# Kernel optimization log

Measured on AMD Instinct MI355X. Metric: run time of the kernel, lower is better.

## Reference

```python
import jax, jax.numpy as jnp
import numpy as np

NU = 100000  # user nodes
NI = 100000  # item nodes
NE = 600000  # edges per etype


def mean_agg(Wh, src, dst, n_dst):
    # copy_u + mean reduce: gather projected src feats, segment-mean over dst
    msg = Wh[src]                                               # [E, d]
    s = jax.ops.segment_sum(msg, dst, num_segments=n_dst)       # [n_dst, d]
    deg = jax.ops.segment_sum(jnp.ones((src.shape[0],), Wh.dtype), dst,
                              num_segments=n_dst)               # [n_dst]
    return s / jnp.maximum(deg, 1.0)[:, None]                   # isolated nodes -> 0


def setup_inputs() -> dict:
    key = jax.random.key(0)
    ks = jax.random.split(key, 20)
    d_in, d_hid, d_out = 128, 128, 16
    inp = {
        'embed_user': jax.random.normal(ks[0], (NU, d_in), jnp.float32),
        'embed_item': jax.random.normal(ks[1], (NI, d_in), jnp.float32),
        'src_uu': jax.random.randint(ks[2], (NE,), 0, NU, jnp.int32),
        'dst_uu': jax.random.randint(ks[3], (NE,), 0, NU, jnp.int32),
        'src_ui': jax.random.randint(ks[4], (NE,), 0, NU, jnp.int32),
        'dst_ui': jax.random.randint(ks[5], (NE,), 0, NI, jnp.int32),
        'src_iu': jax.random.randint(ks[6], (NE,), 0, NI, jnp.int32),
        'dst_iu': jax.random.randint(ks[7], (NE,), 0, NU, jnp.int32),
        'W0_uu': jax.random.normal(ks[8], (d_in, d_hid), jnp.float32) * 0.05,
        'b0_uu': jax.random.normal(ks[9], (d_hid,), jnp.float32) * 0.05,
        'W0_ui': jax.random.normal(ks[10], (d_in, d_hid), jnp.float32) * 0.05,
        'b0_ui': jax.random.normal(ks[11], (d_hid,), jnp.float32) * 0.05,
        'W0_iu': jax.random.normal(ks[12], (d_in, d_hid), jnp.float32) * 0.05,
        'b0_iu': jax.random.normal(ks[13], (d_hid,), jnp.float32) * 0.05,
        'W1_uu': jax.random.normal(ks[14], (d_hid, d_out), jnp.float32) * 0.05,
        'b1_uu': jax.random.normal(ks[15], (d_out,), jnp.float32) * 0.05,
        'W1_ui': jax.random.normal(ks[16], (d_hid, d_out), jnp.float32) * 0.05,
        'b1_ui': jax.random.normal(ks[17], (d_out,), jnp.float32) * 0.05,
        'W1_iu': jax.random.normal(ks[18], (d_hid, d_out), jnp.float32) * 0.05,
        'b1_iu': jax.random.normal(ks[19], (d_out,), jnp.float32) * 0.05,
    }
    return inp


def reference(embed_user, embed_item,
              src_uu, dst_uu, src_ui, dst_ui, src_iu, dst_iu,
              W0_uu, b0_uu, W0_ui, b0_ui, W0_iu, b0_iu,
              W1_uu, b1_uu, W1_ui, b1_ui, W1_iu, b1_iu):
    # Layer 0: per-etype linear, copy_u+mean per etype, sum-combine per dst ntype
    h_user = (mean_agg(embed_user @ W0_uu + b0_uu, src_uu, dst_uu, NU)
              + mean_agg(embed_item @ W0_iu + b0_iu, src_iu, dst_iu, NU))
    h_item = mean_agg(embed_user @ W0_ui + b0_ui, src_ui, dst_ui, NI)
    h_user = jax.nn.relu(h_user)
    h_item = jax.nn.relu(h_item)
    # Layer 1 (dropout p=0): only category='user' output is returned
    out = (mean_agg(h_user @ W1_uu + b1_uu, src_uu, dst_uu, NU)
           + mean_agg(h_item @ W1_iu + b1_iu, src_iu, dst_iu, NU))
    return out
```

## Files before the change

kernel.cpp:

```cpp
#include <hip/hip_runtime.h>
#include <hip/hip_bf16.h>

#define NU 100000
#define NI 100000
#define NEDGE 600000
#define DIN 128
#define DOUT 16
#define NPAD 100032
#define BSH 9
#define NBUCK 196
#define NSB 256
#define SCH 2344

typedef __attribute__((ext_vector_type(8))) short short8;
typedef __attribute__((ext_vector_type(4))) float f32x4;

#define W_EU   0ull
#define W_AUI  6400000ull
#define W_AUU  12802048ull
#define W_AIU  19204096ull
#define W_PW   25606144ull
#define W_OFFU 25632768ull
#define W_OFFI 25732784ull
#define W_OFFX 25832800ull
#define W_SUU  25932816ull
#define W_SIU  26532816ull
#define W_SUI  27132816ull
#define W_EI   27732944ull
#define WS_FULL_BYTES (34132944ull * 4)

__device__ inline unsigned pack_bf16(float x, float y) {
  __hip_bfloat162 h = __float22bfloat162_rn(make_float2(x, y));
  unsigned u;
  __builtin_memcpy(&u, &h, 4);
  return u;
}

__device__ inline short bf16_bits(float x) {
  __hip_bfloat16 h = __float2bfloat16(x);
  short s;
  __builtin_memcpy(&s, &h, 2);
  return s;
}

__device__ inline void bf2_accw(unsigned u, float w, float& ax, float& ay) {
  unsigned lo = u << 16, hi = u & 0xffff0000u;
  float f0, f1;
  __builtin_memcpy(&f0, &lo, 4);
  __builtin_memcpy(&f1, &hi, 4);
  ax = fmaf(f0, w, ax);
  ay = fmaf(f1, w, ay);
}

__global__ __launch_bounds__(256) void prep_kernel(
    const float* __restrict__ Eu, const float* __restrict__ Ei,
    unsigned* __restrict__ Eu_b, unsigned* __restrict__ Ei_b,
    const int* __restrict__ d_uu, const int* __restrict__ d_iu, const int* __restrict__ d_ui,
    int* __restrict__ M,
    const float* __restrict__ W0_uu, const float* __restrict__ W0_ui,
    const float* __restrict__ W0_iu, const float* __restrict__ W1_uu,
    const float* __restrict__ W1_iu, short* __restrict__ pW0_uu, short* __restrict__ pW0_ui,
    short* __restrict__ pW0_iu, short* __restrict__ pW1_uu, short* __restrict__ pW1_iu,
    int nconvU, int nconvI) {
  __shared__ int h[NBUCK];
  int b = blockIdx.x;
  int tid = threadIdx.x;
  if (b < nconvU + nconvI) {
    const float* src;
    unsigned* dst;
    int t;
    if (b < nconvU) { src = Eu; dst = Eu_b; t = b * 256 + tid; }
    else { src = Ei; dst = Ei_b; t = (b - nconvU) * 256 + tid; }
    const float4* s4 = (const float4*)src;
    float4 x = s4[(size_t)t * 2], y = s4[(size_t)t * 2 + 1];
    uint4 o;
    o.x = pack_bf16(x.x, x.y);
    o.y = pack_bf16(x.z, x.w);
    o.z = pack_bf16(y.x, y.y);
    o.w = pack_bf16(y.z, y.w);
    ((uint4*)dst)[t] = o;
    return;
  }
  b -= nconvU + nconvI;
  if (b < 3 * NSB) {
    int t = b / NSB, k = b % NSB;
    if (tid < NBUCK) h[tid] = 0;
    __syncthreads();
    const int* d = (t == 0) ? d_uu : (t == 1) ? d_iu : d_ui;
    int e0 = k * SCH, e1 = min(e0 + SCH, NEDGE);
    for (int e = e0 + tid; e < e1; e += 256) atomicAdd(&h[d[e] >> BSH], 1);
    __syncthreads();
    if (tid < NBUCK) M[t * (NBUCK * NSB) + tid * NSB + k] = h[tid];
    return;
  }
  b -= 3 * NSB;
  int t = b * 256 + tid;
  const float* src;
  short* dst;
  int base;
  bool w1 = false;
  if (t < 16384) { src = W0_uu; dst = pW0_uu; base = t; }
  else if (t < 32768) { src = W0_ui; dst = pW0_ui; base = t - 16384; }
  else if (t < 49152) { src = W0_iu; dst = pW0_iu; base = t - 32768; }
  else if (t < 51200) { src = W1_uu; dst = pW1_uu; base = t - 49152; w1 = true; }
  else if (t < 53248) { src = W1_iu; dst = pW1_iu; base = t - 51200; w1 = true; }
  else return;
  int j = base & 7;
  int lane = (base >> 3) & 63;
  int frag = base >> 9;
  int quad = lane >> 4, l16 = lane & 15;
  float val;
  if (!w1) {
    int kc = frag >> 3, nt = frag & 7;
    val = src[(kc * 32 + quad * 8 + j) * 128 + nt * 16 + l16];
  } else {
    int kc = frag;
    val = src[(kc * 32 + quad * 8 + j) * 16 + l16];
  }
  dst[base] = bf16_bits(val);
}

__global__ __launch_bounds__(256) void scanM_kernel(int* __restrict__ M,
                                                    int* __restrict__ Btot) {
  int t = blockIdx.x / NBUCK, b = blockIdx.x % NBUCK;
  int* Mt = M + t * (NBUCK * NSB) + b * NSB;
  __shared__ int wls[4];
  __shared__ int tot;
  int tid = threadIdx.x, lane = tid & 63, wv = tid >> 6;
  int v = Mt[tid];
  int x = v;
#pragma unroll
  for (int d = 1; d < 64; d <<= 1) {
    int y = __shfl_up(x, d, 64);
    if (lane >= d) x += y;
  }
  if (lane == 63) wls[wv] = x;
  __syncthreads();
  if (tid == 0) {
    int r = 0;
#pragma unroll
    for (int i = 0; i < 4; i++) { int tt = wls[i]; wls[i] = r; r += tt; }
    tot = r;
  }
  __syncthreads();
  Mt[tid] = x - v + wls[wv];
  if (tid == 0) Btot[t * NBUCK + b] = tot;
}

__global__ __launch_bounds__(256) void scanB_kernel(const int* __restrict__ Btot,
                                                    int* __restrict__ Bbase) {
  int t = blockIdx.x;
  __shared__ int wls[4];
  int tid = threadIdx.x, lane = tid & 63, wv = tid >> 6;
  int v = (tid < NBUCK) ? Btot[t * NBUCK + tid] : 0;
  int x = v;
#pragma unroll
  for (int d = 1; d < 64; d <<= 1) {
    int y = __shfl_up(x, d, 64);
    if (lane >= d) x += y;
  }
  if (lane == 63) wls[wv] = x;
  __syncthreads();
  if (tid == 0) {
    int r = 0;
#pragma unroll
    for (int i = 0; i < 4; i++) { int tt = wls[i]; wls[i] = r; r += tt; }
  }
  __syncthreads();
  if (tid < NBUCK) Bbase[t * NBUCK + tid] = x - v + wls[wv];
}

__global__ __launch_bounds__(256) void coarse_scatter_kernel(
    const int* __restrict__ s_uu, const int* __restrict__ d_uu,
    const int* __restrict__ s_iu, const int* __restrict__ d_iu,
    const int* __restrict__ s_ui, const int* __restrict__ d_ui,
    const int* __restrict__ M, const int* __restrict__ Bbase, uint2* __restrict__ pairs) {
  __shared__ int cur[NBUCK];
  int t = blockIdx.x / NSB, k = blockIdx.x % NSB;
  int tid = threadIdx.x;
  if (tid < NBUCK) cur[tid] = M[t * (NBUCK * NSB) + tid * NSB + k] + Bbase[t * NBUCK + tid];
  __syncthreads();
  const int* src = (t == 0) ? s_uu : (t == 1) ? s_iu : s_ui;
  const int* dst = (t == 0) ? d_uu : (t == 1) ? d_iu : d_ui;
  uint2* pr = pairs + (size_t)t * NEDGE;
  int e0 = k * SCH, e1 = min(e0 + SCH, NEDGE);
  for (int e = e0 + tid; e < e1; e += 256) {
    int d = dst[e];
    int pos = atomicAdd(&cur[d >> BSH], 1);
    pr[pos] = make_uint2((unsigned)src[e], (unsigned)d);
  }
}

__global__ __launch_bounds__(256) void fine_sort_kernel(
    const uint2* __restrict__ pairs, const int* __restrict__ Bbase,
    const int* __restrict__ Btot,
    int* __restrict__ off_uu, int* __restrict__ off_iu, int* __restrict__ off_ui,
    int* __restrict__ ssrc_uu, int* __restrict__ ssrc_iu, int* __restrict__ ssrc_ui) {
  __shared__ int h[1 << BSH];
  __shared__ int wls[4];
  int t = blockIdx.x / NBUCK, b = blockIdx.x % NBUCK;
  int tid = threadIdx.x, lane = tid & 63, wv = tid >> 6;
  int* off = (t == 0) ? off_uu : (t == 1) ? off_iu : off_ui;
  int* ss = (t == 0) ? ssrc_uu : (t == 1) ? ssrc_iu : ssrc_ui;
  const uint2* pr = pairs + (size_t)t * NEDGE;
  int base = b << BSH;
  int base_off = Bbase[t * NBUCK + b];
  int cnt = Btot[t * NBUCK + b];
  h[tid] = 0;
  h[tid + 256] = 0;
  __syncthreads();
  for (int e = base_off + tid; e < base_off + cnt; e += 256)
    atomicAdd(&h[(int)pr[e].y - base], 1);
  __syncthreads();
  int h0 = h[2 * tid], h1 = h[2 * tid + 1];
  int s = h0 + h1, x = s;
#pragma unroll
  for (int d = 1; d < 64; d <<= 1) {
    int y = __shfl_up(x, d, 64);
    if (lane >= d) x += y;
  }
  if (lane == 63) wls[wv] = x;
  __syncthreads();
  if (tid == 0) {
    int r = 0;
#pragma unroll
    for (int i = 0; i < 4; i++) { int tt = wls[i]; wls[i] = r; r += tt; }
  }
  __syncthreads();
  int excl = base_off + x - s + wls[wv];
  h[2 * tid] = excl;
  h[2 * tid + 1] = excl + h0;
  __syncthreads();
  int nn = min(1 << BSH, NU - base);
  for (int i = tid; i < nn; i += 256) off[base + i] = h[i];
  if (b == NBUCK - 1 && tid == 0) off[NU] = base_off + cnt;
  __syncthreads();
  for (int e = base_off + tid; e < base_off + cnt; e += 256) {
    uint2 p = pr[e];
    int pos = atomicAdd(&h[(int)p.y - base], 1);
    ss[pos] = (int)p.x;
  }
}

__global__ __launch_bounds__(256) void agg3_kernel(
    const unsigned* __restrict__ Xu, const void* __restrict__ Xi, int xi_bf16,
    const int* __restrict__ off_ui, const int* __restrict__ off_uu, const int* __restrict__ off_iu,
    const int* __restrict__ s_ui, const int* __restrict__ s_uu, const int* __restrict__ s_iu,
    uint4* __restrict__ A_ui, uint4* __restrict__ A_uu, uint4* __restrict__ A_iu, int nb1) {
  int seg = blockIdx.x / nb1;
  int node = (blockIdx.x % nb1) * 16 + (threadIdx.x >> 4);
  int l16 = threadIdx.x & 15;
  const int* off;
  const int* ss;
  uint4* A;
  if (seg == 0) { off = off_ui; ss = s_ui; A = A_ui; }
  else if (seg == 1) { off = off_uu; ss = s_uu; A = A_uu; }
  else { off = off_iu; ss = s_iu; A = A_iu; }
  if (node >= NPAD) return;
  float ac[8];
#pragma unroll
  for (int j = 0; j < 8; j++) ac[j] = 0.f;
  int deg = 0;
  if (node < NU) {
    int s0 = off[node], s1 = off[node + 1];
    deg = s1 - s0;
    if (deg > 0) {
      if (seg < 2 || xi_bf16) {
        const uint4* X = (const uint4*)((seg < 2) ? Xu : (const unsigned*)Xi);
        for (int e = s0; e < s1; e += 8) {
          int idx[8];
          float wt[8];
#pragma unroll
          for (int j = 0; j < 8; j++) {
            int ee = e + j;
            bool v = ee < s1;
            idx[j] = ss[v ? ee : s1 - 1];
            wt[j] = v ? 1.f : 0.f;
          }
          uint4 vv[8];
#pragma unroll
          for (int j = 0; j < 8; j++) vv[j] = X[(size_t)idx[j] * 16 + l16];
#pragma unroll
          for (int j = 0; j < 8; j++) {
            bf2_accw(vv[j].x, wt[j], ac[0], ac[1]);
            bf2_accw(vv[j].y, wt[j], ac[2], ac[3]);
            bf2_accw(vv[j].z, wt[j], ac[4], ac[5]);
            bf2_accw(vv[j].w, wt[j], ac[6], ac[7]);
          }
        }
      } else {
        const float4* Xf = (const float4*)Xi;
        for (int e = s0; e < s1; e += 4) {
          int idx[4];
          float wt[4];
#pragma unroll
          for (int j = 0; j < 4; j++) {
            int ee = e + j;
            bool v = ee < s1;
            idx[j] = ss[v ? ee : s1 - 1];
            wt[j] = v ? 1.f : 0.f;
          }
#pragma unroll
          for (int j = 0; j < 4; j++) {
            float4 pa = Xf[(size_t)idx[j] * 32 + l16 * 2];
            float4 qa = Xf[(size_t)idx[j] * 32 + l16 * 2 + 1];
            ac[0] = fmaf(pa.x, wt[j], ac[0]); ac[1] = fmaf(pa.y, wt[j], ac[1]);
            ac[2] = fmaf(pa.z, wt[j], ac[2]); ac[3] = fmaf(pa.w, wt[j], ac[3]);
            ac[4] = fmaf(qa.x, wt[j], ac[4]); ac[5] = fmaf(qa.y, wt[j], ac[5]);
            ac[6] = fmaf(qa.z, wt[j], ac[6]); ac[7] = fmaf(qa.w, wt[j], ac[7]);
          }
        }
      }
    }
  }
  float inv = 1.0f / fmaxf((float)deg, 1.0f);
  uint4 o;
  o.x = pack_bf16(ac[0] * inv, ac[1] * inv);
  o.y = pack_bf16(ac[2] * inv, ac[3] * inv);
  o.z = pack_bf16(ac[4] * inv, ac[5] * inv);
  o.w = pack_bf16(ac[6] * inv, ac[7] * inv);
  A[(size_t)node * 16 + l16] = o;
}

__global__ __launch_bounds__(256) void rows_mfma_kernel(
    const __hip_bfloat16* __restrict__ A_ui, const __hip_bfloat16* __restrict__ A_uu,
    const __hip_bfloat16* __restrict__ A_iu, const int* __restrict__ off_ui,
    const int* __restrict__ off_uu, const int* __restrict__ off_iu,
    const short* __restrict__ pW0_ui, const short* __restrict__ pW0_uu,
    const short* __restrict__ pW0_iu, const float* __restrict__ b0_ui,
    const float* __restrict__ b0_uu, const float* __restrict__ b0_iu,
    const short* __restrict__ pW1_iu, const short* __restrict__ pW1_uu,
    const float* __restrict__ b1_iu, const float* __restrict__ b1_uu,
    float* __restrict__ P_iu, float* __restrict__ P_uu, int nbi) {
  __shared__ float hs[4][2560];

  const int tid = threadIdx.x;
  const int w = tid >> 6, lane = tid & 63;
  const int quad = lane >> 4, l16 = lane & 15;
  const bool user = (int)blockIdx.x >= nbi;
  const int blk = user ? (int)blockIdx.x - nbi : (int)blockIdx.x;
  const int rb = blk * 64 + w * 16;

  const __hip_bfloat16* A0 = user ? A_uu : A_ui;
  const int* off0 = user ? off_uu : off_ui;
  const short* W0a = user ? pW0_uu : pW0_ui;
  const float* b0a = user ? b0_uu : b0_ui;
  const short* W1p = user ? pW1_uu : pW1_iu;
  const float* b1v = user ? b1_uu : b1_iu;
  float* P = user ? P_uu : P_iu;

  float m0[4], m1[4];
#pragma unroll
  for (int r = 0; r < 4; r++) {
    int rr = rb + quad * 4 + r;
    m0[r] = 0.f;
    m1[r] = 0.f;
    if (rr < NU) {
      m0[r] = (off0[rr + 1] > off0[rr]) ? 1.f : 0.f;
      if (user) m1[r] = (off_iu[rr + 1] > off_iu[rr]) ? 1.f : 0.f;
    }
  }

  f32x4 acc[8];
#pragma unroll
  for (int nt = 0; nt < 8; nt++) {
    float ba = b0a[nt * 16 + l16];
    float bb = user ? b0_iu[nt * 16 + l16] : 0.f;
#pragma unroll
    for (int r = 0; r < 4; r++) acc[nt][r] = ba * m0[r] + bb * m1[r];
  }

  const short8* A0v = (const short8*)(A0 + (size_t)(rb + l16) * DIN);
  const short8* A1v = (const short8*)(A_iu + (size_t)(rb + l16) * DIN);
  const short8* B0p = (const short8*)W0a;
  const short8* B1p = (const short8*)pW0_iu;

#pragma unroll
  for (int kc = 0; kc < 4; kc++) {
    short8 a0 = A0v[kc * 4 + quad];
    short8 a1 = user ? A1v[kc * 4 + quad] : a0;
#pragma unroll
    for (int nt = 0; nt < 8; nt++) {
      short8 b0 = B0p[(kc * 8 + nt) * 64 + lane];
      acc[nt] = __builtin_amdgcn_mfma_f32_16x16x32_bf16(a0, b0, acc[nt], 0, 0, 0);
      if (user) {
        short8 bb = B1p[(kc * 8 + nt) * 64 + lane];
        acc[nt] = __builtin_amdgcn_mfma_f32_16x16x32_bf16(a1, bb, acc[nt], 0, 0, 0);
      }
    }
  }

  float* hw = &hs[w][0];
#pragma unroll
  for (int nt = 0; nt < 8; nt++) {
    int col = nt * 16 + l16;
    float4 v;
    v.x = fmaxf(acc[nt][0], 0.f);
    v.y = fmaxf(acc[nt][1], 0.f);
    v.z = fmaxf(acc[nt][2], 0.f);
    v.w = fmaxf(acc[nt][3], 0.f);
    *(float4*)&hw[col * 20 + quad * 4] = v;
  }
  __syncthreads();

  f32x4 acc2;
  {
    float bv = b1v[l16];
    acc2[0] = bv; acc2[1] = bv; acc2[2] = bv; acc2[3] = bv;
  }
  const short8* W1f = (const short8*)W1p;
#pragma unroll
  for (int kc = 0; kc < 4; kc++) {
    float f[8];
#pragma unroll
    for (int j = 0; j < 8; j++) f[j] = hw[(kc * 32 + quad * 8 + j) * 20 + l16];
    union { uint4 u; short8 s; } hf;
    hf.u.x = pack_bf16(f[0], f[1]);
    hf.u.y = pack_bf16(f[2], f[3]);
    hf.u.z = pack_bf16(f[4], f[5]);
    hf.u.w = pack_bf16(f[6], f[7]);
    short8 bw = W1f[kc * 64 + lane];
    acc2 = __builtin_amdgcn_mfma_f32_16x16x32_bf16(hf.s, bw, acc2, 0, 0, 0);
  }
#pragma unroll
  for (int r = 0; r < 4; r++) {
    int rr = rb + quad * 4 + r;
    if (rr < NU) P[(size_t)rr * DOUT + l16] = acc2[r];
  }
}

__global__ __launch_bounds__(256) void out_kernel(const float4* __restrict__ P_uu,
                                                  const float4* __restrict__ P_iu,
                                                  const int* __restrict__ off_uu,
                                                  const int* __restrict__ s_uu,
                                                  const int* __restrict__ off_iu,
                                                  const int* __restrict__ s_iu,
                                                  float4* __restrict__ out) {
  int w = threadIdx.x >> 6, lane = threadIdx.x & 63;
  int q = lane & 3;
  int sl = (lane >> 2) & 3;
  int nl = lane >> 4;
  int node = blockIdx.x * 16 + w * 4 + nl;
  float4 a = make_float4(0.f, 0.f, 0.f, 0.f);
  float4 b = a;
  int s0 = off_uu[node], s1 = off_uu[node + 1];
  for (int e = s0 + sl; e < s1; e += 4) {
    float4 v = P_uu[(size_t)s_uu[e] * 4 + q];
    a.x += v.x; a.y += v.y; a.z += v.z; a.w += v.w;
  }
  int t0 = off_iu[node], t1 = off_iu[node + 1];
  for (int e = t0 + sl; e < t1; e += 4) {
    float4 v = P_iu[(size_t)s_iu[e] * 4 + q];
    b.x += v.x; b.y += v.y; b.z += v.z; b.w += v.w;
  }
  float ia = 1.0f / fmaxf((float)(s1 - s0), 1.0f);
  float ib = 1.0f / fmaxf((float)(t1 - t0), 1.0f);
  float4 r;
  r.x = a.x * ia + b.x * ib;
  r.y = a.y * ia + b.y * ib;
  r.z = a.z * ia + b.z * ib;
  r.w = a.w * ia + b.w * ib;
  r.x += __shfl_xor(r.x, 4, 64); r.y += __shfl_xor(r.y, 4, 64);
  r.z += __shfl_xor(r.z, 4, 64); r.w += __shfl_xor(r.w, 4, 64);
  r.x += __shfl_xor(r.x, 8, 64); r.y += __shfl_xor(r.y, 8, 64);
  r.z += __shfl_xor(r.z, 8, 64); r.w += __shfl_xor(r.w, 8, 64);
  if (sl == 0) out[(size_t)node * 4 + q] = r;
}

extern "C" void kernel_launch(void* const* d_in, const int* in_sizes, int n_in,
                              void* d_out, int out_size, void* d_ws, size_t ws_size,
                              hipStream_t stream) {
  (void)in_sizes; (void)n_in; (void)out_size;
  const float* embed_user = (const float*)d_in[0];
  const float* embed_item = (const float*)d_in[1];
  const int* src_uu = (const int*)d_in[2];
  const int* dst_uu = (const int*)d_in[3];
  const int* src_ui = (const int*)d_in[4];
  const int* dst_ui = (const int*)d_in[5];
  const int* src_iu = (const int*)d_in[6];
  const int* dst_iu = (const int*)d_in[7];
  const float* W0_uu = (const float*)d_in[8];
  const float* b0_uu = (const float*)d_in[9];
  const float* W0_ui = (const float*)d_in[10];
  const float* b0_ui = (const float*)d_in[11];
  const float* W0_iu = (const float*)d_in[12];
  const float* b0_iu = (const float*)d_in[13];
  const float* W1_uu = (const float*)d_in[14];
  const float* b1_uu = (const float*)d_in[15];
  const float* W1_iu = (const float*)d_in[18];
  const float* b1_iu = (const float*)d_in[19];
  float* out = (float*)d_out;

  char* ws = (char*)d_ws;
  unsigned* Eu_b = (unsigned*)(ws + W_EU * 4);
  unsigned* A_ui = (unsigned*)(ws + W_AUI * 4);
  unsigned* A_uu = (unsigned*)(ws + W_AUU * 4);
  unsigned* A_iu = (unsigned*)(ws + W_AIU * 4);
  short* pW0_uu = (short*)(ws + W_PW * 4);
  short* pW0_ui = pW0_uu + 16384;
  short* pW0_iu = pW0_uu + 32768;
  short* pW1_uu = pW0_uu + 49152;
  short* pW1_iu = pW0_uu + 51200;
  int* off_uu = (int*)(ws + W_OFFU * 4);
  int* off_iu = (int*)(ws + W_OFFI * 4);
  int* off_ui = (int*)(ws + W_OFFX * 4);
  int* ssrc_uu = (int*)(ws + W_SUU * 4);
  int* ssrc_iu = (int*)(ws + W_SIU * 4);
  int* ssrc_ui = (int*)(ws + W_SUI * 4);
  unsigned* Ei_b = (unsigned*)(ws + W_EI * 4);
  uint2* pairs = (uint2*)A_ui;
  int* M = (int*)A_uu;
  int* Btot = M + NBUCK * NSB * 3;
  int* Bbase = Btot + NBUCK * 3;
  float* P_iu = (float*)Eu_b;
  float* P_uu = P_iu + 1600000;

  const int full = (ws_size >= WS_FULL_BYTES) ? 1 : 0;
  const int nconvU = 6250, nconvI = full ? 6250 : 0;
  const void* Xi = full ? (const void*)Ei_b : (const void*)embed_item;

  prep_kernel<<<nconvU + nconvI + 3 * NSB + 208, 256, 0, stream>>>(
      embed_user, embed_item, Eu_b, Ei_b, dst_uu, dst_iu, dst_ui, M,
      W0_uu, W0_ui, W0_iu, W1_uu, W1_iu, pW0_uu, pW0_ui, pW0_iu, pW1_uu, pW1_iu,
      nconvU, nconvI);

  scanM_kernel<<<3 * NBUCK, 256, 0, stream>>>(M, Btot);
  scanB_kernel<<<3, 256, 0, stream>>>(Btot, Bbase);
  coarse_scatter_kernel<<<3 * NSB, 256, 0, stream>>>(src_uu, dst_uu, src_iu, dst_iu,
                                                     src_ui, dst_ui, M, Bbase, pairs);
  fine_sort_kernel<<<3 * NBUCK, 256, 0, stream>>>(pairs, Bbase, Btot,
                                                  off_uu, off_iu, off_ui,
                                                  ssrc_uu, ssrc_iu, ssrc_ui);

  const int nb1 = NPAD / 16;
  agg3_kernel<<<3 * nb1, 256, 0, stream>>>(Eu_b, Xi, full, off_ui, off_uu, off_iu,
                                           ssrc_ui, ssrc_uu, ssrc_iu,
                                           (uint4*)A_ui, (uint4*)A_uu, (uint4*)A_iu, nb1);

  const int nbi = NPAD / 64;
  rows_mfma_kernel<<<2 * nbi, 256, 0, stream>>>(
      (const __hip_bfloat16*)A_ui, (const __hip_bfloat16*)A_uu, (const __hip_bfloat16*)A_iu,
      off_ui, off_uu, off_iu, pW0_ui, pW0_uu, pW0_iu, b0_ui, b0_uu, b0_iu,
      pW1_iu, pW1_uu, b1_iu, b1_uu, P_iu, P_uu, nbi);

  out_kernel<<<NU / 16, 256, 0, stream>>>((const float4*)P_uu, (const float4*)P_iu,
                                          off_uu, ssrc_uu, off_iu, ssrc_iu,
                                          (float4*)out);
}
```

Before: 376.0 us.

## Fuse layer-0 gather-mean aggregation into the MFMA row kernel via LDS staging

Merges the separate aggregation kernel into the per-row MFMA kernel. Each wave now gathers and mean-aggregates its 16 rows into an XOR-swizzled LDS tile, then feeds the MFMA directly from LDS, removing the global write and re-read of the three aggregated bf16 feature matrices and one launch. The tradeoff is lower gather parallelism per block: each 16-lane group processes 4 nodes serially, and user blocks do two passes. An extra barrier is also needed before LDS is reused for the hidden activations.

```diff
diff --git a/kernel.cpp b/kernel.cpp
--- a/kernel.cpp
+++ b/kernel.cpp
@@ -242,106 +242,108 @@
   }
 }
 
-__global__ __launch_bounds__(256) void agg3_kernel(
-    const unsigned* __restrict__ Xu, const void* __restrict__ Xi, int xi_bf16,
+__global__ __launch_bounds__(256) void fused_layer_kernel(
+    const uint4* __restrict__ Xu4, const void* __restrict__ Xi, int xi_bf16,
     const int* __restrict__ off_ui, const int* __restrict__ off_uu, const int* __restrict__ off_iu,
     const int* __restrict__ s_ui, const int* __restrict__ s_uu, const int* __restrict__ s_iu,
-    uint4* __restrict__ A_ui, uint4* __restrict__ A_uu, uint4* __restrict__ A_iu, int nb1) {
-  int seg = blockIdx.x / nb1;
-  int node = (blockIdx.x % nb1) * 16 + (threadIdx.x >> 4);
-  int l16 = threadIdx.x & 15;
-  const int* off;
-  const int* ss;
-  uint4* A;
-  if (seg == 0) { off = off_ui; ss = s_ui; A = A_ui; }
-  else if (seg == 1) { off = off_uu; ss = s_uu; A = A_uu; }
-  else { off = off_iu; ss = s_iu; A = A_iu; }
-  if (node >= NPAD) return;
-  float ac[8];
-#pragma unroll
-  for (int j = 0; j < 8; j++) ac[j] = 0.f;
-  int deg = 0;
-  if (node < NU) {
-    int s0 = off[node], s1 = off[node + 1];
-    deg = s1 - s0;
-    if (deg > 0) {
-      if (seg < 2 || xi_bf16) {
-        const uint4* X = (const uint4*)((seg < 2) ? Xu : (const unsigned*)Xi);
-        for (int e = s0; e < s1; e += 8) {
-          int idx[8];
-          float wt[8];
-#pragma unroll
-          for (int j = 0; j < 8; j++) {
-            int ee = e + j;
-            bool v = ee < s1;
-            idx[j] = ss[v ? ee : s1 - 1];
-            wt[j] = v ? 1.f : 0.f;
-          }
-          uint4 vv[8];
-#pragma unroll
-          for (int j = 0; j < 8; j++) vv[j] = X[(size_t)idx[j] * 16 + l16];
-#pragma unroll
-          for (int j = 0; j < 8; j++) {
-            bf2_accw(vv[j].x, wt[j], ac[0], ac[1]);
-            bf2_accw(vv[j].y, wt[j], ac[2], ac[3]);
-            bf2_accw(vv[j].z, wt[j], ac[4], ac[5]);
-            bf2_accw(vv[j].w, wt[j], ac[6], ac[7]);
-          }
-        }
-      } else {
-        const float4* Xf = (const float4*)Xi;
-        for (int e = s0; e < s1; e += 4) {
-          int idx[4];
-          float wt[4];
-#pragma unroll
-          for (int j = 0; j < 4; j++) {
-            int ee = e + j;
-            bool v = ee < s1;
-            idx[j] = ss[v ? ee : s1 - 1];
-            wt[j] = v ? 1.f : 0.f;
-          }
-#pragma unroll
-          for (int j = 0; j < 4; j++) {
-            float4 pa = Xf[(size_t)idx[j] * 32 + l16 * 2];
-            float4 qa = Xf[(size_t)idx[j] * 32 + l16 * 2 + 1];
-            ac[0] = fmaf(pa.x, wt[j], ac[0]); ac[1] = fmaf(pa.y, wt[j], ac[1]);
-            ac[2] = fmaf(pa.z, wt[j], ac[2]); ac[3] = fmaf(pa.w, wt[j], ac[3]);
-            ac[4] = fmaf(qa.x, wt[j], ac[4]); ac[5] = fmaf(qa.y, wt[j], ac[5]);
-            ac[6] = fmaf(qa.z, wt[j], ac[6]); ac[7] = fmaf(qa.w, wt[j], ac[7]);
-          }
-        }
-      }
-    }
-  }
-  float inv = 1.0f / fmaxf((float)deg, 1.0f);
-  uint4 o;
-  o.x = pack_bf16(ac[0] * inv, ac[1] * inv);
-  o.y = pack_bf16(ac[2] * inv, ac[3] * inv);
-  o.z = pack_bf16(ac[4] * inv, ac[5] * inv);
-  o.w = pack_bf16(ac[6] * inv, ac[7] * inv);
-  A[(size_t)node * 16 + l16] = o;
-}
-
-__global__ __launch_bounds__(256) void rows_mfma_kernel(
-    const __hip_bfloat16* __restrict__ A_ui, const __hip_bfloat16* __restrict__ A_uu,
-    const __hip_bfloat16* __restrict__ A_iu, const int* __restrict__ off_ui,
-    const int* __restrict__ off_uu, const int* __restrict__ off_iu,
     const short* __restrict__ pW0_ui, const short* __restrict__ pW0_uu,
     const short* __restrict__ pW0_iu, const float* __restrict__ b0_ui,
     const float* __restrict__ b0_uu, const float* __restrict__ b0_iu,
     const short* __restrict__ pW1_iu, const short* __restrict__ pW1_uu,
     const float* __restrict__ b1_iu, const float* __restrict__ b1_uu,
     float* __restrict__ P_iu, float* __restrict__ P_uu, int nbi) {
-  __shared__ float hs[4][2560];
+  __shared__ __align__(16) float hs[4][2560];
 
   const int tid = threadIdx.x;
   const int w = tid >> 6, lane = tid & 63;
-  const int quad = lane >> 4, l16 = lane & 15;
   const bool user = (int)blockIdx.x >= nbi;
   const int blk = user ? (int)blockIdx.x - nbi : (int)blockIdx.x;
   const int rb = blk * 64 + w * 16;
 
-  const __hip_bfloat16* A0 = user ? A_uu : A_ui;
+  float* hw = &hs[w][0];
+  uint4* A0 = (uint4*)hw;
+  uint4* A1 = A0 + 256;
+
+  {
+    const int g = (tid >> 4) & 3, l16 = tid & 15;
+    const int npass = user ? 2 : 1;
+    for (int pass = 0; pass < npass; pass++) {
+      const int* off = pass ? off_iu : (user ? off_uu : off_ui);
+      const int* ss = pass ? s_iu : (user ? s_uu : s_ui);
+      uint4* A = pass ? A1 : A0;
+      const bool bf = pass ? (xi_bf16 != 0) : true;
+      const uint4* X = pass ? (const uint4*)Xi : Xu4;
+      const float4* Xf = (const float4*)Xi;
+      for (int it = 0; it < 4; it++) {
+        int r = g * 4 + it;
+        int node = rb + r;
+        float ac[8];
+#pragma unroll
+        for (int j = 0; j < 8; j++) ac[j] = 0.f;
+        int deg = 0;
+        if (node < NU) {
+          int s0 = off[node], s1 = off[node + 1];
+          deg = s1 - s0;
+          if (deg > 0) {
+            if (bf) {
+              for (int e = s0; e < s1; e += 8) {
+                int idx[8];
+                float wt[8];
+#pragma unroll
+                for (int j = 0; j < 8; j++) {
+                  int ee = e + j;
+                  bool v = ee < s1;
+                  idx[j] = ss[v ? ee : s1 - 1];
+                  wt[j] = v ? 1.f : 0.f;
+                }
+                uint4 vv[8];
+#pragma unroll
+                for (int j = 0; j < 8; j++) vv[j] = X[(size_t)idx[j] * 16 + l16];
+#pragma unroll
+                for (int j = 0; j < 8; j++) {
+                  bf2_accw(vv[j].x, wt[j], ac[0], ac[1]);
+                  bf2_accw(vv[j].y, wt[j], ac[2], ac[3]);
+                  bf2_accw(vv[j].z, wt[j], ac[4], ac[5]);
+                  bf2_accw(vv[j].w, wt[j], ac[6], ac[7]);
+                }
+              }
+            } else {
+              for (int e = s0; e < s1; e += 4) {
+                int idx[4];
+                float wt[4];
+#pragma unroll
+                for (int j = 0; j < 4; j++) {
+                  int ee = e + j;
+                  bool v = ee < s1;
+                  idx[j] = ss[v ? ee : s1 - 1];
+                  wt[j] = v ? 1.f : 0.f;
+                }
+#pragma unroll
+                for (int j = 0; j < 4; j++) {
+                  float4 pa = Xf[(size_t)idx[j] * 32 + l16 * 2];
+                  float4 qa = Xf[(size_t)idx[j] * 32 + l16 * 2 + 1];
+                  ac[0] = fmaf(pa.x, wt[j], ac[0]); ac[1] = fmaf(pa.y, wt[j], ac[1]);
+                  ac[2] = fmaf(pa.z, wt[j], ac[2]); ac[3] = fmaf(pa.w, wt[j], ac[3]);
+                  ac[4] = fmaf(qa.x, wt[j], ac[4]); ac[5] = fmaf(qa.y, wt[j], ac[5]);
+                  ac[6] = fmaf(qa.z, wt[j], ac[6]); ac[7] = fmaf(qa.w, wt[j], ac[7]);
+                }
+              }
+            }
+          }
+        }
+        float inv = 1.0f / fmaxf((float)deg, 1.0f);
+        uint4 o;
+        o.x = pack_bf16(ac[0] * inv, ac[1] * inv);
+        o.y = pack_bf16(ac[2] * inv, ac[3] * inv);
+        o.z = pack_bf16(ac[4] * inv, ac[5] * inv);
+        o.w = pack_bf16(ac[6] * inv, ac[7] * inv);
+        A[r * 16 + (l16 ^ (r & 7))] = o;
+      }
+    }
+  }
+  __syncthreads();
+
+  const int quad = lane >> 4, q16 = lane & 15;
   const int* off0 = user ? off_uu : off_ui;
   const short* W0a = user ? pW0_uu : pW0_ui;
   const float* b0a = user ? b0_uu : b0_ui;
@@ -364,36 +366,36 @@
   f32x4 acc[8];
 #pragma unroll
   for (int nt = 0; nt < 8; nt++) {
-    float ba = b0a[nt * 16 + l16];
-    float bb = user ? b0_iu[nt * 16 + l16] : 0.f;
+    float ba = b0a[nt * 16 + q16];
+    float bb = user ? b0_iu[nt * 16 + q16] : 0.f;
 #pragma unroll
     for (int r = 0; r < 4; r++) acc[nt][r] = ba * m0[r] + bb * m1[r];
   }
 
-  const short8* A0v = (const short8*)(A0 + (size_t)(rb + l16) * DIN);
-  const short8* A1v = (const short8*)(A_iu + (size_t)(rb + l16) * DIN);
   const short8* B0p = (const short8*)W0a;
   const short8* B1p = (const short8*)pW0_iu;
-
+  union u4s8 { uint4 u; short8 s; };
 #pragma unroll
   for (int kc = 0; kc < 4; kc++) {
-    short8 a0 = A0v[kc * 4 + quad];
-    short8 a1 = user ? A1v[kc * 4 + quad] : a0;
+    int c = kc * 4 + quad;
+    u4s8 a0, a1;
+    a0.u = A0[q16 * 16 + (c ^ (q16 & 7))];
+    if (user) a1.u = A1[q16 * 16 + (c ^ (q16 & 7))];
 #pragma unroll
     for (int nt = 0; nt < 8; nt++) {
       short8 b0 = B0p[(kc * 8 + nt) * 64 + lane];
-      acc[nt] = __builtin_amdgcn_mfma_f32_16x16x32_bf16(a0, b0, acc[nt], 0, 0, 0);
+      acc[nt] = __builtin_amdgcn_mfma_f32_16x16x32_bf16(a0.s, b0, acc[nt], 0, 0, 0);
       if (user) {
         short8 bb = B1p[(kc * 8 + nt) * 64 + lane];
-        acc[nt] = __builtin_amdgcn_mfma_f32_16x16x32_bf16(a1, bb, acc[nt], 0, 0, 0);
+        acc[nt] = __builtin_amdgcn_mfma_f32_16x16x32_bf16(a1.s, bb, acc[nt], 0, 0, 0);
       }
     }
   }
-
-  float* hw = &hs[w][0];
+  __syncthreads();
+
 #pragma unroll
   for (int nt = 0; nt < 8; nt++) {
-    int col = nt * 16 + l16;
+    int col = nt * 16 + q16;
     float4 v;
     v.x = fmaxf(acc[nt][0], 0.f);
     v.y = fmaxf(acc[nt][1], 0.f);
@@ -405,7 +407,7 @@
 
   f32x4 acc2;
   {
-    float bv = b1v[l16];
+    float bv = b1v[q16];
     acc2[0] = bv; acc2[1] = bv; acc2[2] = bv; acc2[3] = bv;
   }
   const short8* W1f = (const short8*)W1p;
@@ -413,7 +415,7 @@
   for (int kc = 0; kc < 4; kc++) {
     float f[8];
 #pragma unroll
-    for (int j = 0; j < 8; j++) f[j] = hw[(kc * 32 + quad * 8 + j) * 20 + l16];
+    for (int j = 0; j < 8; j++) f[j] = hw[(kc * 32 + quad * 8 + j) * 20 + q16];
     union { uint4 u; short8 s; } hf;
     hf.u.x = pack_bf16(f[0], f[1]);
     hf.u.y = pack_bf16(f[2], f[3]);
@@ -425,7 +427,7 @@
 #pragma unroll
   for (int r = 0; r < 4; r++) {
     int rr = rb + quad * 4 + r;
-    if (rr < NU) P[(size_t)rr * DOUT + l16] = acc2[r];
+    if (rr < NU) P[(size_t)rr * DOUT + q16] = acc2[r];
   }
 }
 
@@ -493,9 +495,6 @@
 
   char* ws = (char*)d_ws;
   unsigned* Eu_b = (unsigned*)(ws + W_EU * 4);
-  unsigned* A_ui = (unsigned*)(ws + W_AUI * 4);
-  unsigned* A_uu = (unsigned*)(ws + W_AUU * 4);
-  unsigned* A_iu = (unsigned*)(ws + W_AIU * 4);
   short* pW0_uu = (short*)(ws + W_PW * 4);
   short* pW0_ui = pW0_uu + 16384;
   short* pW0_iu = pW0_uu + 32768;
@@ -508,11 +507,11 @@
   int* ssrc_iu = (int*)(ws + W_SIU * 4);
   int* ssrc_ui = (int*)(ws + W_SUI * 4);
   unsigned* Ei_b = (unsigned*)(ws + W_EI * 4);
-  uint2* pairs = (uint2*)A_ui;
-  int* M = (int*)A_uu;
+  uint2* pairs = (uint2*)(ws + W_AUI * 4);
+  int* M = (int*)(ws + W_AUU * 4);
   int* Btot = M + NBUCK * NSB * 3;
   int* Bbase = Btot + NBUCK * 3;
-  float* P_iu = (float*)Eu_b;
+  float* P_iu = (float*)(ws + W_AUU * 4);
   float* P_uu = P_iu + 1600000;
 
   const int full = (ws_size >= WS_FULL_BYTES) ? 1 : 0;
@@ -532,15 +531,11 @@
                                                   off_uu, off_iu, off_ui,
                                                   ssrc_uu, ssrc_iu, ssrc_ui);
 
-  const int nb1 = NPAD / 16;
-  agg3_kernel<<<3 * nb1, 256, 0, stream>>>(Eu_b, Xi, full, off_ui, off_uu, off_iu,
-                                           ssrc_ui, ssrc_uu, ssrc_iu,
-                                           (uint4*)A_ui, (uint4*)A_uu, (uint4*)A_iu, nb1);
-
   const int nbi = NPAD / 64;
-  rows_mfma_kernel<<<2 * nbi, 256, 0, stream>>>(
-      (const __hip_bfloat16*)A_ui, (const __hip_bfloat16*)A_uu, (const __hip_bfloat16*)A_iu,
-      off_ui, off_uu, off_iu, pW0_ui, pW0_uu, pW0_iu, b0_ui, b0_uu, b0_iu,
+  fused_layer_kernel<<<2 * nbi, 256, 0, stream>>>(
+      (const uint4*)Eu_b, Xi, full, off_ui, off_uu, off_iu,
+      ssrc_ui, ssrc_uu, ssrc_iu,
+      pW0_ui, pW0_uu, pW0_iu, b0_ui, b0_uu, b0_iu,
       pW1_iu, pW1_uu, b1_iu, b1_uu, P_iu, P_uu, nbi);
 
   out_kernel<<<NU / 16, 256, 0, stream>>>((const float4*)P_uu, (const float4*)P_iu,
```

Result: faster. 355.2 us (-5.5%).
